# Performance work log

Measured on AMD Instinct MI355X. Metric: run time of the kernel, lower is better.

## Reference

```python
import jax, jax.numpy as jnp
import numpy as np

H = 8  # num_heads


def _ln(x, g, b):
    mu = x.mean(-1, keepdims=True)
    var = ((x - mu) ** 2).mean(-1, keepdims=True)
    return (x - mu) * jax.lax.rsqrt(var + 1e-5) * g + b


def setup_inputs() -> dict:
    key = jax.random.key(0)
    ks = jax.random.split(key, 24)
    B, N, V, E, D, R, L = 8, 512, 50000, 300, 256, 100, 4
    dh = D // H
    s = 0.02
    inp = {}
    inp['token_ids'] = jax.random.randint(ks[0], (B, N), 0, V, dtype=jnp.int32)
    inp['relations'] = jax.random.randint(ks[1], (B, N, N), 0, R, dtype=jnp.int32)
    m = jax.random.bernoulli(ks[2], 0.9, (B, N, N))
    eye = jnp.eye(N, dtype=bool)[None]
    inp['relations_mask'] = jnp.logical_or(m, eye)  # keep diagonal valid so every row attends somewhere
    inp['embed'] = jax.random.normal(ks[3], (V, E), jnp.float32) * s
    inp['W_in'] = jax.random.normal(ks[4], (E, D), jnp.float32) * s
    inp['b_in'] = jnp.zeros((D,), jnp.float32)
    inp['Wq'] = jax.random.normal(ks[5], (L, D, D), jnp.float32) * s
    inp['Wk'] = jax.random.normal(ks[6], (L, D, D), jnp.float32) * s
    inp['Wv'] = jax.random.normal(ks[7], (L, D, D), jnp.float32) * s
    inp['Wo'] = jax.random.normal(ks[8], (L, D, D), jnp.float32) * s
    inp['ln1_g'] = jnp.ones((L, D), jnp.float32)
    inp['ln1_b'] = jnp.zeros((L, D), jnp.float32)
    inp['ln2_g'] = jnp.ones((L, D), jnp.float32)
    inp['ln2_b'] = jnp.zeros((L, D), jnp.float32)
    inp['W1'] = jax.random.normal(ks[9], (L, D, 4 * D), jnp.float32) * s
    inp['b1'] = jnp.zeros((L, 4 * D), jnp.float32)
    inp['W2'] = jax.random.normal(ks[10], (L, 4 * D, D), jnp.float32) * s
    inp['b2'] = jnp.zeros((L, D), jnp.float32)
    inp['rel_k_emb'] = jax.random.normal(ks[11], (R, dh), jnp.float32) * s
    inp['rel_v_emb'] = jax.random.normal(ks[12], (R, dh), jnp.float32) * s
    inp['W_out'] = jax.random.normal(ks[13], (D, D), jnp.float32) * s
    inp['b_out'] = jnp.zeros((D,), jnp.float32)
    return inp


def reference(token_ids, relations, relations_mask, embed, W_in, b_in, Wq, Wk, Wv, Wo,
              ln1_g, ln1_b, ln2_g, ln2_b, W1, b1, W2, b2, rel_k_emb, rel_v_emb, W_out, b_out):
    # Input layer: embedding lookup + projection to gnn hidden size.
    x = embed[token_ids]                          # [B,N,E]
    x = jax.nn.relu(x @ W_in + b_in)              # [B,N,D]
    B, N, D = x.shape
    dh = D // H
    # Shared relation embeddings (share_layers=True, share_heads=True): gathered once.
    rk = rel_k_emb[relations]                     # [B,N,N,dh]
    rv = rel_v_emb[relations]                     # [B,N,N,dh]
    neg = jnp.asarray(-1e9, x.dtype)
    scale = jnp.asarray(1.0 / np.sqrt(dh), x.dtype)
    L = Wq.shape[0]
    for l in range(L):  # fixed small layer count
        q = (x @ Wq[l]).reshape(B, N, H, dh).transpose(0, 2, 1, 3)
        k = (x @ Wk[l]).reshape(B, N, H, dh).transpose(0, 2, 1, 3)
        v = (x @ Wv[l]).reshape(B, N, H, dh).transpose(0, 2, 1, 3)
        # Relation-aware scores: q.k + q.r_k (RAT-SQL)
        scores = (jnp.einsum('bhnd,bhmd->bhnm', q, k)
                  + jnp.einsum('bhnd,bnmd->bhnm', q, rk)) * scale
        scores = jnp.where(relations_mask[:, None], scores, neg)
        a = jax.nn.softmax(scores, axis=-1)       # [B,H,N,N]
        z = (jnp.einsum('bhnm,bhmd->bhnd', a, v)
             + jnp.einsum('bhnm,bnmd->bhnd', a, rv))
        z = z.transpose(0, 2, 1, 3).reshape(B, N, D) @ Wo[l]
        x = _ln(x + z, ln1_g[l], ln1_b[l])
        f = jax.nn.relu(x @ W1[l] + b1[l]) @ W2[l] + b2[l]
        x = _ln(x + f, ln2_g[l], ln2_b[l])
    # Output layer projection
    return x @ W_out + b_out
```

## Files before the change

### kernel.cpp

```cpp
#include <hip/hip_runtime.h>
#include <hip/hip_bf16.h>

#define NTOK 4096
#define NN   512

typedef __attribute__((ext_vector_type(8))) short bf16x8;
typedef __attribute__((ext_vector_type(4))) short bf16x4;
typedef __attribute__((ext_vector_type(4))) float f32x4;

__device__ __forceinline__ float bf16_to_f(unsigned short u) {
    unsigned int x = ((unsigned int)u) << 16;
    return __builtin_bit_cast(float, x);
}
__device__ __forceinline__ unsigned short f_to_bf16(float f) {
    unsigned int b = __builtin_bit_cast(unsigned int, f);
    return (unsigned short)((b + 0x7fff + ((b >> 16) & 1)) >> 16);
}
__device__ __forceinline__ bf16x8 pack8(float4 a, float4 b) {
    bf16x8 v;
    v[0]=(short)f_to_bf16(a.x); v[1]=(short)f_to_bf16(a.y);
    v[2]=(short)f_to_bf16(a.z); v[3]=(short)f_to_bf16(a.w);
    v[4]=(short)f_to_bf16(b.x); v[5]=(short)f_to_bf16(b.y);
    v[6]=(short)f_to_bf16(b.z); v[7]=(short)f_to_bf16(b.w);
    return v;
}

__global__ void detect_mask_kernel(const unsigned char* __restrict__ m, int* __restrict__ flag) {
    __shared__ int f;
    if (threadIdx.x == 0) f = 0;
    __syncthreads();
    int any = 0;
    for (int i = threadIdx.x; i < 4096; i += 256) {
        if ((i & 3) != 0 && m[i] != 0) any = 1;
    }
    if (any) atomicOr(&f, 1);
    __syncthreads();
    if (threadIdx.x == 0) *flag = f;
}

__global__ __launch_bounds__(256) void prep_rel16(
    const int* __restrict__ rel, const void* __restrict__ mask,
    const int* __restrict__ flag, short* __restrict__ rel16)
{
    const bool mbyte = (*flag != 0);
    const unsigned char* m8 = (const unsigned char*)mask;
    const int* m32 = (const int*)mask;
    const int i = (blockIdx.x * 256 + threadIdx.x) * 2;
    int2 rv = *(const int2*)(rel + i);
    int ok0, ok1;
    if (mbyte) { ok0 = m8[i]; ok1 = m8[i + 1]; }
    else       { ok0 = (m32[i] != 0); ok1 = (m32[i + 1] != 0); }
    short2 o;
    o.x = ok0 ? (short)rv.x : (short)-1;
    o.y = ok1 ? (short)rv.y : (short)-1;
    *(short2*)(rel16 + i) = o;
}

__global__ __launch_bounds__(256) void embed_proj_kernel(
    const int* __restrict__ tok, const float* __restrict__ embed,
    const float* __restrict__ W_in, const float* __restrict__ b_in,
    float* __restrict__ x)
{
    __shared__ float emb[8][304];
    __shared__ int tloc[8];
    const int t = threadIdx.x;
    const int r0 = blockIdx.x * 8;
    if (t < 8) tloc[t] = tok[r0 + t];
    __syncthreads();
    for (int i = t; i < 8 * 300; i += 256) {
        int r = i / 300, e = i - r * 300;
        emb[r][e] = embed[(size_t)tloc[r] * 300 + e];
    }
    __syncthreads();
    float acc[8] = {0.f,0.f,0.f,0.f,0.f,0.f,0.f,0.f};
    const int d = t;
    for (int e = 0; e < 300; ++e) {
        float w = W_in[e * 256 + d];
#pragma unroll
        for (int r = 0; r < 8; ++r) acc[r] += emb[r][e] * w;
    }
    const float bb = b_in[d];
#pragma unroll
    for (int r = 0; r < 8; ++r) {
        float o = acc[r] + bb;
        o = o > 0.f ? o : 0.f;
        x[(size_t)(r0 + r) * 256 + d] = o;
    }
}

__global__ __launch_bounds__(256) void gemm_mfma(
    const float* __restrict__ A,
    const float* __restrict__ W0, const float* __restrict__ W1p, const float* __restrict__ W2p,
    int ncPerW, const float* __restrict__ bias,
    float* __restrict__ C, int M, int K, int Nc, int relu)
{
    __shared__ unsigned short As[2][64][40];
    __shared__ unsigned short Bs[2][64][40];

    const int t = threadIdx.x;
    const int lane = t & 63, w = t >> 6;
    const int g = lane >> 4, li = lane & 15;
    const int r0 = blockIdx.y * 64, c0 = blockIdx.x * 64;

    const float* Wp = W0; int cW = c0;
    if (c0 >= 2 * ncPerW)      { Wp = W2p; cW = c0 - 2 * ncPerW; }
    else if (c0 >= ncPerW)     { Wp = W1p; cW = c0 - ncPerW; }

    f32x4 acc[4];
#pragma unroll
    for (int i = 0; i < 4; ++i) acc[i] = (f32x4){0.f, 0.f, 0.f, 0.f};

    const int arow = t >> 2, ad8 = (t & 3) * 8;
    const int bnn = t & 63, bk8 = (t >> 6) * 8;

    const float* ap0 = A + (size_t)(r0 + arow) * K + ad8;
    float4 a0 = *(const float4*)ap0;
    float4 a1 = *(const float4*)(ap0 + 4);
    float wv[8];
#pragma unroll
    for (int j = 0; j < 8; ++j)
        wv[j] = Wp[(size_t)(bk8 + j) * ncPerW + cW + bnn];

    const int nk = K >> 5;
    for (int ki = 0; ki < nk; ++ki) {
        const int cur = ki & 1;
        *(bf16x8*)&As[cur][arow][ad8] = pack8(a0, a1);
        {
            bf16x8 v;
#pragma unroll
            for (int j = 0; j < 8; ++j) v[j] = (short)f_to_bf16(wv[j]);
            *(bf16x8*)&Bs[cur][bnn][bk8] = v;
        }
        if (ki + 1 < nk) {
            const int k0 = (ki + 1) * 32;
            const float* ap = A + (size_t)(r0 + arow) * K + k0 + ad8;
            a0 = *(const float4*)ap;
            a1 = *(const float4*)(ap + 4);
#pragma unroll
            for (int j = 0; j < 8; ++j)
                wv[j] = Wp[(size_t)(k0 + bk8 + j) * ncPerW + cW + bnn];
        }
        __syncthreads();
        bf16x8 af = *(const bf16x8*)&As[cur][16 * w + li][g * 8];
#pragma unroll
        for (int sub = 0; sub < 4; ++sub) {
            bf16x8 bfr = *(const bf16x8*)&Bs[cur][16 * sub + li][g * 8];
            acc[sub] = __builtin_amdgcn_mfma_f32_16x16x32_bf16(af, bfr, acc[sub], 0, 0, 0);
        }
    }
#pragma unroll
    for (int sub = 0; sub < 4; ++sub) {
        int col = c0 + sub * 16 + li;
        float bv = bias ? bias[col] : 0.f;
#pragma unroll
        for (int r = 0; r < 4; ++r) {
            int row = r0 + 16 * w + g * 4 + r;
            float o = acc[sub][r] + bv;
            if (relu) o = fmaxf(o, 0.f);
            C[(size_t)row * Nc + col] = o;
        }
    }
}

__global__ __launch_bounds__(256, 3) void attn_mfma(
    const float* __restrict__ qkv,
    const short* __restrict__ rel16,
    const float* __restrict__ relk_g,
    const float* __restrict__ relv_g,
    float* __restrict__ zpart,
    float* __restrict__ smpart)
{
    const int p = blockIdx.x;
    const int cx = p & 7, kk = p >> 3;
    const int sg = cx * 32 + (kk >> 3);
    const int h  = kk & 7;
    const int b = sg >> 5, chunk = (sg >> 2) & 7, ms = sg & 3;
    const int n0 = chunk * 64, mbase = ms * 128;

    const int t = threadIdx.x;
    const int lane = t & 63, w = t >> 6;
    const int g = lane >> 4, li = lane & 15;
    const int qrow = 16 * w + g * 4;

    __shared__ float wrel[64][100];
    __shared__ unsigned short qrk[64][100];
    __shared__ union {
        unsigned short relk_s[100][40];
        unsigned short relvT[32][136];
        struct {
            unsigned short v_t[2][32][40];
            unsigned short p_s[4][16][40];
        } mn;
    } u;

    for (int i = t; i < 6400; i += 256) ((float*)wrel)[i] = 0.f;
    for (int i = t; i < 400; i += 256) {
        int rr = i >> 2, d8 = (i & 3) * 8;
        const float* sp = relk_g + rr * 32 + d8;
        *(bf16x8*)&u.relk_s[rr][d8] = pack8(*(const float4*)sp, *(const float4*)(sp + 4));
    }
    const float scale = 0.17677669529663687f;
    bf16x8 qf;
    {
        const float* qp = qkv + (size_t)(b * NN + n0 + 16 * w + li) * 768 + h * 32 + g * 8;
        float4 q0 = *(const float4*)qp, q1 = *(const float4*)(qp + 4);
        q0.x *= scale; q0.y *= scale; q0.z *= scale; q0.w *= scale;
        q1.x *= scale; q1.y *= scale; q1.z *= scale; q1.w *= scale;
        qf = pack8(q0, q1);
    }

    const short* relrow[4];
#pragma unroll
    for (int r = 0; r < 4; ++r)
        relrow[r] = rel16 + ((size_t)b * NN + n0 + qrow + r) * NN;
    const int vm = t & 31, vdg = t >> 5;
    const size_t kRB = (size_t)(b * NN) * 768 + 256 + h * 32 + g * 8;
    const size_t vRB = (size_t)(b * NN) * 768 + 512 + h * 32 + vdg * 4;

    float4 kld[4][4]; float4 vld[4]; short rld[4][8];
    {
        const int m0 = mbase;
        kld[0][0] = *(const float4*)(qkv + kRB + (size_t)(m0 + li) * 768);
        kld[0][1] = *(const float4*)(qkv + kRB + (size_t)(m0 + li) * 768 + 4);
        kld[0][2] = *(const float4*)(qkv + kRB + (size_t)(m0 + 16 + li) * 768);
        kld[0][3] = *(const float4*)(qkv + kRB + (size_t)(m0 + 16 + li) * 768 + 4);
        vld[0]    = *(const float4*)(qkv + vRB + (size_t)(m0 + vm) * 768);
#pragma unroll
        for (int idx = 0; idx < 8; ++idx)
            rld[0][idx] = relrow[idx & 3][m0 + (idx >> 2) * 16 + li];
    }
    __syncthreads();

#pragma unroll
    for (int rc = 0; rc < 7; ++rc) {
        bf16x8 bb = *(const bf16x8*)&u.relk_s[rc * 16 + li][g * 8];
        f32x4 s = __builtin_amdgcn_mfma_f32_16x16x32_bf16(qf, bb, (f32x4){0.f,0.f,0.f,0.f}, 0, 0, 0);
        int col = rc * 16 + li;
        if (col < 100) {
#pragma unroll
            for (int r = 0; r < 4; ++r)
                qrk[qrow + r][col] = f_to_bf16(s[r]);
        }
    }
    __syncthreads();

    float smacc[4] = {0.f, 0.f, 0.f, 0.f};
    f32x4 zf[2];
    zf[0] = (f32x4){0.f,0.f,0.f,0.f};
    zf[1] = (f32x4){0.f,0.f,0.f,0.f};

#pragma unroll
    for (int tt = 0; tt < 4; ++tt) {
        const int cur = tt & 1;
        {
            float4 vv = vld[tt];
            u.mn.v_t[cur][vdg * 4 + 0][vm] = f_to_bf16(vv.x);
            u.mn.v_t[cur][vdg * 4 + 1][vm] = f_to_bf16(vv.y);
            u.mn.v_t[cur][vdg * 4 + 2][vm] = f_to_bf16(vv.z);
            u.mn.v_t[cur][vdg * 4 + 3][vm] = f_to_bf16(vv.w);
        }
        __syncthreads();
        bf16x8 kf0 = pack8(kld[tt][0], kld[tt][1]);
        bf16x8 kf1 = pack8(kld[tt][2], kld[tt][3]);
        short rcur[8];
#pragma unroll
        for (int idx = 0; idx < 8; ++idx) rcur[idx] = rld[tt][idx];
        if (tt + 1 < 4) {
            const int m0n = mbase + (tt + 1) * 32;
            kld[tt+1][0] = *(const float4*)(qkv + kRB + (size_t)(m0n + li) * 768);
            kld[tt+1][1] = *(const float4*)(qkv + kRB + (size_t)(m0n + li) * 768 + 4);
            kld[tt+1][2] = *(const float4*)(qkv + kRB + (size_t)(m0n + 16 + li) * 768);
            kld[tt+1][3] = *(const float4*)(qkv + kRB + (size_t)(m0n + 16 + li) * 768 + 4);
            vld[tt+1]    = *(const float4*)(qkv + vRB + (size_t)(m0n + vm) * 768);
#pragma unroll
            for (int idx = 0; idx < 8; ++idx)
                rld[tt+1][idx] = relrow[idx & 3][m0n + (idx >> 2) * 16 + li];
        }
        f32x4 s0 = __builtin_amdgcn_mfma_f32_16x16x32_bf16(qf, kf0, (f32x4){0.f,0.f,0.f,0.f}, 0, 0, 0);
        f32x4 s1 = __builtin_amdgcn_mfma_f32_16x16x32_bf16(qf, kf1, (f32x4){0.f,0.f,0.f,0.f}, 0, 0, 0);
        float pr[8];
#pragma unroll
        for (int idx = 0; idx < 8; ++idx) {
            const int r = idx & 3;
            const int rl = rcur[idx];
            const int rla = rl < 0 ? 0 : rl;
            const float qadd = bf16_to_f(qrk[qrow + r][rla]);
            const float sv = ((idx >> 2) ? s1[r] : s0[r]) + qadd;
            float pv = 0.f;
            if (rl >= 0) {
                pv = __expf(fminf(sv, 50.f));
                atomicAdd(&wrel[qrow + r][rl], pv);
            }
            smacc[r] += pv;
            pr[idx] = pv;
        }
#pragma unroll
        for (int idx = 0; idx < 8; ++idx)
            u.mn.p_s[w][g * 4 + (idx & 3)][(idx >> 2) * 16 + li] = f_to_bf16(pr[idx]);

        asm volatile("s_waitcnt lgkmcnt(0)" ::: "memory");
        __builtin_amdgcn_sched_barrier(0);
        bf16x8 pa = *(const bf16x8*)&u.mn.p_s[w][li][g * 8];
#pragma unroll
        for (int dc = 0; dc < 2; ++dc) {
            bf16x8 vb = *(const bf16x8*)&u.mn.v_t[cur][dc * 16 + li][g * 8];
            zf[dc] = __builtin_amdgcn_mfma_f32_16x16x32_bf16(pa, vb, zf[dc], 0, 0, 0);
        }
    }
    __syncthreads();

    for (int i = t; i < 32 * 36; i += 256) {
        int d = i / 36, c = 100 + (i - (i / 36) * 36);
        u.relvT[d][c] = 0;
    }
    for (int i = t; i < 400; i += 256) {
        int rr2 = i >> 2, d8 = (i & 3) * 8;
        const float* sp = relv_g + rr2 * 32 + d8;
        float4 s0 = *(const float4*)sp, s1 = *(const float4*)(sp + 4);
        u.relvT[d8 + 0][rr2] = f_to_bf16(s0.x);
        u.relvT[d8 + 1][rr2] = f_to_bf16(s0.y);
        u.relvT[d8 + 2][rr2] = f_to_bf16(s0.z);
        u.relvT[d8 + 3][rr2] = f_to_bf16(s0.w);
        u.relvT[d8 + 4][rr2] = f_to_bf16(s1.x);
        u.relvT[d8 + 5][rr2] = f_to_bf16(s1.y);
        u.relvT[d8 + 6][rr2] = f_to_bf16(s1.z);
        u.relvT[d8 + 7][rr2] = f_to_bf16(s1.w);
    }
    __syncthreads();

#pragma unroll
    for (int kc = 0; kc < 4; ++kc) {
        const int kbase = kc * 32 + g * 8;
        const float* wp = &wrel[16 * w + li][0];
        bf16x8 af;
#pragma unroll
        for (int j = 0; j < 8; ++j) {
            int idx = kbase + j;
            float val = (idx < 100) ? wp[idx] : 0.f;
            af[j] = (short)f_to_bf16(val);
        }
#pragma unroll
        for (int dc = 0; dc < 2; ++dc) {
            bf16x8 vb = *(const bf16x8*)&u.relvT[dc * 16 + li][kbase];
            zf[dc] = __builtin_amdgcn_mfma_f32_16x16x32_bf16(af, vb, zf[dc], 0, 0, 0);
        }
    }

#pragma unroll
    for (int r = 0; r < 4; ++r) {
        smacc[r] += __shfl_xor(smacc[r], 1, 64);
        smacc[r] += __shfl_xor(smacc[r], 2, 64);
        smacc[r] += __shfl_xor(smacc[r], 4, 64);
        smacc[r] += __shfl_xor(smacc[r], 8, 64);
    }
#pragma unroll
    for (int r = 0; r < 4; ++r) {
        const int row = b * NN + n0 + qrow + r;
        size_t ob = (size_t)ms * 1048576 + (size_t)row * 256 + h * 32;
#pragma unroll
        for (int dc = 0; dc < 2; ++dc)
            zpart[ob + dc * 16 + li] = zf[dc][r];
        if (li == 0)
            smpart[(size_t)ms * 32768 + (size_t)row * 8 + h] = smacc[r];
    }
}

__global__ __launch_bounds__(256) void combine_kernel(
    const float* __restrict__ zpart, const float* __restrict__ smpart,
    float* __restrict__ z)
{
    const int t = threadIdx.x;
    const int wi = t >> 6, lane = t & 63;
    const int row = blockIdx.x * 4 + wi;
    const int h = lane >> 3;
    float den = 0.f;
    float4 acc = make_float4(0.f, 0.f, 0.f, 0.f);
#pragma unroll
    for (int s = 0; s < 4; ++s) {
        den += smpart[(size_t)s * 32768 + (size_t)row * 8 + h];
        float4 v = *(const float4*)(zpart + (size_t)s * 1048576 + (size_t)row * 256 + lane * 4);
        acc.x += v.x; acc.y += v.y; acc.z += v.z; acc.w += v.w;
    }
    const float inv = 1.f / den;
    acc.x *= inv; acc.y *= inv; acc.z *= inv; acc.w *= inv;
    *(float4*)(z + (size_t)row * 256 + lane * 4) = acc;
}

__global__ __launch_bounds__(256) void ln_kernel(
    const float* __restrict__ xin, const float* __restrict__ y,
    const float* __restrict__ g, const float* __restrict__ bsh,
    float* __restrict__ xout)
{
    const int t = threadIdx.x;
    const int w = t >> 6, lane = t & 63;
    const size_t row = (size_t)blockIdx.x * 4 + w;
    const float4 xv = *(const float4*)(xin + row * 256 + lane * 4);
    const float4 yv = *(const float4*)(y + row * 256 + lane * 4);
    float4 sv;
    sv.x = xv.x + yv.x; sv.y = xv.y + yv.y; sv.z = xv.z + yv.z; sv.w = xv.w + yv.w;
    float sum = sv.x + sv.y + sv.z + sv.w;
    float sq  = sv.x * sv.x + sv.y * sv.y + sv.z * sv.z + sv.w * sv.w;
#pragma unroll
    for (int off = 1; off < 64; off <<= 1) {
        sum += __shfl_xor(sum, off, 64);
        sq  += __shfl_xor(sq, off, 64);
    }
    const float mu = sum * (1.f / 256.f);
    const float var = sq * (1.f / 256.f) - mu * mu;
    const float rs = rsqrtf(var + 1e-5f);
    const float4 gv = *(const float4*)(g + lane * 4);
    const float4 bv = *(const float4*)(bsh + lane * 4);
    float4 o;
    o.x = (sv.x - mu) * rs * gv.x + bv.x;
    o.y = (sv.y - mu) * rs * gv.y + bv.y;
    o.z = (sv.z - mu) * rs * gv.z + bv.z;
    o.w = (sv.w - mu) * rs * gv.w + bv.w;
    *(float4*)(xout + row * 256 + lane * 4) = o;
}

extern "C" void kernel_launch(void* const* d_in, const int* in_sizes, int n_in,
                              void* d_out, int out_size, void* d_ws, size_t ws_size,
                              hipStream_t stream)
{
    (void)in_sizes; (void)n_in; (void)out_size;
    const int*   tok   = (const int*)d_in[0];
    const int*   rel   = (const int*)d_in[1];
    const void*  mask  = d_in[2];
    const float* embed = (const float*)d_in[3];
    const float* W_in  = (const float*)d_in[4];
    const float* b_in  = (const float*)d_in[5];
    const float* Wq    = (const float*)d_in[6];
    const float* Wk    = (const float*)d_in[7];
    const float* Wv    = (const float*)d_in[8];
    const float* Wo    = (const float*)d_in[9];
    const float* ln1g  = (const float*)d_in[10];
    const float* ln1b  = (const float*)d_in[11];
    const float* ln2g  = (const float*)d_in[12];
    const float* ln2b  = (const float*)d_in[13];
    const float* W1    = (const float*)d_in[14];
    const float* b1    = (const float*)d_in[15];
    const float* W2    = (const float*)d_in[16];
    const float* b2    = (const float*)d_in[17];
    const float* relk  = (const float*)d_in[18];
    const float* relv  = (const float*)d_in[19];
    const float* Wout  = (const float*)d_in[20];
    const float* bout  = (const float*)d_in[21];
    float* out = (float*)d_out;

    float* ws  = (float*)d_ws;
    float* x   = ws;
    float* z   = ws + (1u << 20);
    float* zo  = ws + 2u * (1u << 20);
    float* qkv = ws + 3u * (1u << 20);
    float* hb  = ws + 6u * (1u << 20);

    const bool roomy = ws_size >= ((size_t)45 << 20);
    short* rel16 = roomy ? (short*)(ws + 10u * (1u << 20)) : (short*)z;
    int*   flag  = (int*)(ws + (roomy ? 11u : 10u) * (1u << 20));
    float* zpart = hb;
    float* smpart = zo;

    detect_mask_kernel<<<1, 256, 0, stream>>>((const unsigned char*)mask, flag);
    if (roomy)
        prep_rel16<<<4096, 256, 0, stream>>>(rel, mask, flag, rel16);
    embed_proj_kernel<<<512, 256, 0, stream>>>(tok, embed, W_in, b_in, x);

    for (int l = 0; l < 4; ++l) {
        const float* wq = Wq + (size_t)l * 65536;
        const float* wk = Wk + (size_t)l * 65536;
        const float* wv = Wv + (size_t)l * 65536;
        const float* wo = Wo + (size_t)l * 65536;
        const float* w1 = W1 + (size_t)l * 262144;
        const float* w2 = W2 + (size_t)l * 262144;

        if (!roomy)
            prep_rel16<<<4096, 256, 0, stream>>>(rel, mask, flag, rel16);

        gemm_mfma<<<dim3(12, 64), 256, 0, stream>>>(x, wq, wk, wv, 256, nullptr,
                                                    qkv, NTOK, 256, 768, 0);
        attn_mfma<<<2048, 256, 0, stream>>>(qkv, rel16, relk, relv, zpart, smpart);
        combine_kernel<<<1024, 256, 0, stream>>>(zpart, smpart, z);
        gemm_mfma<<<dim3(4, 64), 256, 0, stream>>>(z, wo, wo, wo, 256, nullptr,
                                                   zo, NTOK, 256, 256, 0);
        ln_kernel<<<1024, 256, 0, stream>>>(x, zo, ln1g + l * 256, ln1b + l * 256, x);
        gemm_mfma<<<dim3(16, 64), 256, 0, stream>>>(x, w1, w1, w1, 1024, b1 + l * 1024,
                                                    hb, NTOK, 256, 1024, 1);
        gemm_mfma<<<dim3(4, 64), 256, 0, stream>>>(hb, w2, w2, w2, 256, b2 + l * 256,
                                                   zo, NTOK, 1024, 256, 0);
        ln_kernel<<<1024, 256, 0, stream>>>(x, zo, ln2g + l * 256, ln2b + l * 256, x);
    }
    gemm_mfma<<<dim3(4, 64), 256, 0, stream>>>(x, Wout, Wout, Wout, 256, bout,
                                               out, NTOK, 256, 256, 0);
}
```

Measured before the change: 702.8 us.

## Precompute q·relk globally, halve attention key splits, add 128-row GEMM tile

The per-block q·rel_k product moves out of the attention kernel into a separate qrk_kernel that writes bf16 results to a global buffer. Each attention block now covers 256 keys in 8 steps instead of 128 in 4, which halves the block count and lets combine_kernel sum 2 partials instead of 4. The attention kernel drops its qrk LDS table and asks for 4 blocks per SM. A new 128x64-tile GEMM is used for the QKV and FFN1 projections to improve operand reuse. The cost is an extra launch and a global gather of qrk values per score element, in place of an LDS lookup.

Result: no change. 705.9 us (+0.4%).

```diff
diff --git a/kernel.cpp b/kernel.cpp
--- a/kernel.cpp
+++ b/kernel.cpp
@@ -162,42 +162,105 @@
     }
 }
 
-__global__ __launch_bounds__(256, 3) void attn_mfma(
-    const float* __restrict__ qkv,
-    const short* __restrict__ rel16,
-    const float* __restrict__ relk_g,
-    const float* __restrict__ relv_g,
-    float* __restrict__ zpart,
-    float* __restrict__ smpart)
-{
-    const int p = blockIdx.x;
-    const int cx = p & 7, kk = p >> 3;
-    const int sg = cx * 32 + (kk >> 3);
-    const int h  = kk & 7;
-    const int b = sg >> 5, chunk = (sg >> 2) & 7, ms = sg & 3;
-    const int n0 = chunk * 64, mbase = ms * 128;
+__global__ __launch_bounds__(256) void gemm_mfma_128(
+    const float* __restrict__ A,
+    const float* __restrict__ W0, const float* __restrict__ W1p, const float* __restrict__ W2p,
+    int ncPerW, const float* __restrict__ bias,
+    float* __restrict__ C, int M, int K, int Nc, int relu)
+{
+    __shared__ unsigned short As[2][128][40];
+    __shared__ unsigned short Bs[2][64][40];
 
     const int t = threadIdx.x;
     const int lane = t & 63, w = t >> 6;
     const int g = lane >> 4, li = lane & 15;
+    const int r0 = blockIdx.y * 128, c0 = blockIdx.x * 64;
+
+    const float* Wp = W0; int cW = c0;
+    if (c0 >= 2 * ncPerW)      { Wp = W2p; cW = c0 - 2 * ncPerW; }
+    else if (c0 >= ncPerW)     { Wp = W1p; cW = c0 - ncPerW; }
+
+    f32x4 acc[2][4];
+#pragma unroll
+    for (int i = 0; i < 2; ++i)
+#pragma unroll
+        for (int j = 0; j < 4; ++j) acc[i][j] = (f32x4){0.f, 0.f, 0.f, 0.f};
+
+    const int arow = t >> 1, ah = (t & 1) * 16;
+    const int bnn = t & 63, bk8 = (t >> 6) * 8;
+
+    const float* ap0 = A + (size_t)(r0 + arow) * K + ah;
+    float4 a0 = *(const float4*)ap0;
+    float4 a1 = *(const float4*)(ap0 + 4);
+    float4 a2 = *(const float4*)(ap0 + 8);
+    float4 a3 = *(const float4*)(ap0 + 12);
+    float wv[8];
+#pragma unroll
+    for (int j = 0; j < 8; ++j)
+        wv[j] = Wp[(size_t)(bk8 + j) * ncPerW + cW + bnn];
+
+    const int nk = K >> 5;
+    for (int ki = 0; ki < nk; ++ki) {
+        const int cur = ki & 1;
+        *(bf16x8*)&As[cur][arow][ah]     = pack8(a0, a1);
+        *(bf16x8*)&As[cur][arow][ah + 8] = pack8(a2, a3);
+        {
+            bf16x8 v;
+#pragma unroll
+            for (int j = 0; j < 8; ++j) v[j] = (short)f_to_bf16(wv[j]);
+            *(bf16x8*)&Bs[cur][bnn][bk8] = v;
+        }
+        if (ki + 1 < nk) {
+            const int k0 = (ki + 1) * 32;
+            const float* ap = A + (size_t)(r0 + arow) * K + k0 + ah;
+            a0 = *(const float4*)ap;
+            a1 = *(const float4*)(ap + 4);
+            a2 = *(const float4*)(ap + 8);
+            a3 = *(const float4*)(ap + 12);
+#pragma unroll
+            for (int j = 0; j < 8; ++j)
+                wv[j] = Wp[(size_t)(k0 + bk8 + j) * ncPerW + cW + bnn];
+        }
+        __syncthreads();
+        bf16x8 af0 = *(const bf16x8*)&As[cur][32 * w + li][g * 8];
+        bf16x8 af1 = *(const bf16x8*)&As[cur][32 * w + 16 + li][g * 8];
+#pragma unroll
+        for (int sub = 0; sub < 4; ++sub) {
+            bf16x8 bfr = *(const bf16x8*)&Bs[cur][16 * sub + li][g * 8];
+            acc[0][sub] = __builtin_amdgcn_mfma_f32_16x16x32_bf16(af0, bfr, acc[0][sub], 0, 0, 0);
+            acc[1][sub] = __builtin_amdgcn_mfma_f32_16x16x32_bf16(af1, bfr, acc[1][sub], 0, 0, 0);
+        }
+    }
+#pragma unroll
+    for (int rc = 0; rc < 2; ++rc)
+#pragma unroll
+    for (int sub = 0; sub < 4; ++sub) {
+        int col = c0 + sub * 16 + li;
+        float bv = bias ? bias[col] : 0.f;
+#pragma unroll
+        for (int r = 0; r < 4; ++r) {
+            int row = r0 + 32 * w + rc * 16 + g * 4 + r;
+            float o = acc[rc][sub][r] + bv;
+            if (relu) o = fmaxf(o, 0.f);
+            C[(size_t)row * Nc + col] = o;
+        }
+    }
+}
+
+__global__ __launch_bounds__(256) void qrk_kernel(
+    const float* __restrict__ qkv, const float* __restrict__ relk_g,
+    unsigned short* __restrict__ qrkg)
+{
+    const int n0 = blockIdx.x * 64, h = blockIdx.y, b = blockIdx.z;
+    const int t = threadIdx.x, lane = t & 63, w = t >> 6;
+    const int g = lane >> 4, li = lane & 15;
     const int qrow = 16 * w + g * 4;
 
-    __shared__ float wrel[64][100];
-    __shared__ unsigned short qrk[64][100];
-    __shared__ union {
-        unsigned short relk_s[100][40];
-        unsigned short relvT[32][136];
-        struct {
-            unsigned short v_t[2][32][40];
-            unsigned short p_s[4][16][40];
-        } mn;
-    } u;
-
-    for (int i = t; i < 6400; i += 256) ((float*)wrel)[i] = 0.f;
+    __shared__ unsigned short relk_s[100][40];
     for (int i = t; i < 400; i += 256) {
         int rr = i >> 2, d8 = (i & 3) * 8;
         const float* sp = relk_g + rr * 32 + d8;
-        *(bf16x8*)&u.relk_s[rr][d8] = pack8(*(const float4*)sp, *(const float4*)(sp + 4));
+        *(bf16x8*)&relk_s[rr][d8] = pack8(*(const float4*)sp, *(const float4*)(sp + 4));
     }
     const float scale = 0.17677669529663687f;
     bf16x8 qf;
@@ -208,96 +271,148 @@
         q1.x *= scale; q1.y *= scale; q1.z *= scale; q1.w *= scale;
         qf = pack8(q0, q1);
     }
-
+    __syncthreads();
+#pragma unroll
+    for (int rc = 0; rc < 7; ++rc) {
+        bf16x8 bb = *(const bf16x8*)&relk_s[rc * 16 + li][g * 8];
+        f32x4 s = __builtin_amdgcn_mfma_f32_16x16x32_bf16(qf, bb, (f32x4){0.f,0.f,0.f,0.f}, 0, 0, 0);
+        int col = rc * 16 + li;
+        if (col < 100) {
+#pragma unroll
+            for (int r = 0; r < 4; ++r)
+                qrkg[((size_t)(b * 8 + h) * NN + n0 + qrow + r) * 100 + col] = f_to_bf16(s[r]);
+        }
+    }
+}
+
+__global__ __launch_bounds__(256, 4) void attn_mfma(
+    const float* __restrict__ qkv,
+    const short* __restrict__ rel16,
+    const unsigned short* __restrict__ qrkg,
+    const float* __restrict__ relv_g,
+    float* __restrict__ zpart,
+    float* __restrict__ smpart)
+{
+    const int p = blockIdx.x;
+    const int cx = p & 7, idx0 = p >> 3;
+    const int sg = cx * 8 + (idx0 >> 4);
+    const int hm = idx0 & 15;
+    const int h = hm >> 1, ms = hm & 1;
+    const int b = sg >> 3, chunk = sg & 7;
+    const int n0 = chunk * 64, mbase = ms * 256;
+
+    const int t = threadIdx.x;
+    const int lane = t & 63, w = t >> 6;
+    const int g = lane >> 4, li = lane & 15;
+    const int qrow = 16 * w + g * 4;
+
+    __shared__ float wrel[64][100];
+    __shared__ union {
+        unsigned short relvT[32][136];
+        struct {
+            unsigned short v_t[2][32][40];
+            unsigned short p_s[4][16][40];
+        } mn;
+    } u;
+
+    for (int i = t; i < 6400; i += 256) ((float*)wrel)[i] = 0.f;
+    const float scale = 0.17677669529663687f;
+    bf16x8 qf;
+    {
+        const float* qp = qkv + (size_t)(b * NN + n0 + 16 * w + li) * 768 + h * 32 + g * 8;
+        float4 q0 = *(const float4*)qp, q1 = *(const float4*)(qp + 4);
+        q0.x *= scale; q0.y *= scale; q0.z *= scale; q0.w *= scale;
+        q1.x *= scale; q1.y *= scale; q1.z *= scale; q1.w *= scale;
+        qf = pack8(q0, q1);
+    }
     const short* relrow[4];
-#pragma unroll
-    for (int r = 0; r < 4; ++r)
+    const unsigned short* qgr[4];
+#pragma unroll
+    for (int r = 0; r < 4; ++r) {
         relrow[r] = rel16 + ((size_t)b * NN + n0 + qrow + r) * NN;
+        qgr[r] = qrkg + ((size_t)(b * 8 + h) * NN + n0 + qrow + r) * 100;
+    }
     const int vm = t & 31, vdg = t >> 5;
     const size_t kRB = (size_t)(b * NN) * 768 + 256 + h * 32 + g * 8;
     const size_t vRB = (size_t)(b * NN) * 768 + 512 + h * 32 + vdg * 4;
 
-    float4 kld[4][4]; float4 vld[4]; short rld[4][8];
+    float4 kbuf[2][4]; float4 vbuf[2];
+    short rbuf[2][8]; unsigned short qvb[2][8];
     {
-        const int m0 = mbase;
-        kld[0][0] = *(const float4*)(qkv + kRB + (size_t)(m0 + li) * 768);
-        kld[0][1] = *(const float4*)(qkv + kRB + (size_t)(m0 + li) * 768 + 4);
-        kld[0][2] = *(const float4*)(qkv + kRB + (size_t)(m0 + 16 + li) * 768);
-        kld[0][3] = *(const float4*)(qkv + kRB + (size_t)(m0 + 16 + li) * 768 + 4);
-        vld[0]    = *(const float4*)(qkv + vRB + (size_t)(m0 + vm) * 768);
-#pragma unroll
-        for (int idx = 0; idx < 8; ++idx)
-            rld[0][idx] = relrow[idx & 3][m0 + (idx >> 2) * 16 + li];
-    }
-    __syncthreads();
-
-#pragma unroll
-    for (int rc = 0; rc < 7; ++rc) {
-        bf16x8 bb = *(const bf16x8*)&u.relk_s[rc * 16 + li][g * 8];
-        f32x4 s = __builtin_amdgcn_mfma_f32_16x16x32_bf16(qf, bb, (f32x4){0.f,0.f,0.f,0.f}, 0, 0, 0);
-        int col = rc * 16 + li;
-        if (col < 100) {
-#pragma unroll
-            for (int r = 0; r < 4; ++r)
-                qrk[qrow + r][col] = f_to_bf16(s[r]);
-        }
-    }
-    __syncthreads();
-
+#pragma unroll
+        for (int i = 0; i < 8; ++i)
+            rbuf[0][i] = relrow[i & 3][mbase + (i >> 2) * 16 + li];
+        kbuf[0][0] = *(const float4*)(qkv + kRB + (size_t)(mbase + li) * 768);
+        kbuf[0][1] = *(const float4*)(qkv + kRB + (size_t)(mbase + li) * 768 + 4);
+        kbuf[0][2] = *(const float4*)(qkv + kRB + (size_t)(mbase + 16 + li) * 768);
+        kbuf[0][3] = *(const float4*)(qkv + kRB + (size_t)(mbase + 16 + li) * 768 + 4);
+        vbuf[0]    = *(const float4*)(qkv + vRB + (size_t)(mbase + vm) * 768);
+#pragma unroll
+        for (int i = 0; i < 8; ++i) {
+            int rl = rbuf[0][i];
+            qvb[0][i] = qgr[i & 3][rl < 0 ? 0 : rl];
+        }
+    }
     float smacc[4] = {0.f, 0.f, 0.f, 0.f};
     f32x4 zf[2];
     zf[0] = (f32x4){0.f,0.f,0.f,0.f};
     zf[1] = (f32x4){0.f,0.f,0.f,0.f};
 
-#pragma unroll
-    for (int tt = 0; tt < 4; ++tt) {
-        const int cur = tt & 1;
+    __syncthreads();
+
+#pragma unroll
+    for (int tt = 0; tt < 8; ++tt) {
+        const int cur = tt & 1, nxt = cur ^ 1;
         {
-            float4 vv = vld[tt];
+            float4 vv = vbuf[cur];
             u.mn.v_t[cur][vdg * 4 + 0][vm] = f_to_bf16(vv.x);
             u.mn.v_t[cur][vdg * 4 + 1][vm] = f_to_bf16(vv.y);
             u.mn.v_t[cur][vdg * 4 + 2][vm] = f_to_bf16(vv.z);
             u.mn.v_t[cur][vdg * 4 + 3][vm] = f_to_bf16(vv.w);
         }
+        if (tt + 1 < 8) {
+            const int m0n = mbase + (tt + 1) * 32;
+#pragma unroll
+            for (int i = 0; i < 8; ++i)
+                rbuf[nxt][i] = relrow[i & 3][m0n + (i >> 2) * 16 + li];
+        }
         __syncthreads();
-        bf16x8 kf0 = pack8(kld[tt][0], kld[tt][1]);
-        bf16x8 kf1 = pack8(kld[tt][2], kld[tt][3]);
-        short rcur[8];
-#pragma unroll
-        for (int idx = 0; idx < 8; ++idx) rcur[idx] = rld[tt][idx];
-        if (tt + 1 < 4) {
+        bf16x8 kf0 = pack8(kbuf[cur][0], kbuf[cur][1]);
+        bf16x8 kf1 = pack8(kbuf[cur][2], kbuf[cur][3]);
+        if (tt + 1 < 8) {
             const int m0n = mbase + (tt + 1) * 32;
-            kld[tt+1][0] = *(const float4*)(qkv + kRB + (size_t)(m0n + li) * 768);
-            kld[tt+1][1] = *(const float4*)(qkv + kRB + (size_t)(m0n + li) * 768 + 4);
-            kld[tt+1][2] = *(const float4*)(qkv + kRB + (size_t)(m0n + 16 + li) * 768);
-            kld[tt+1][3] = *(const float4*)(qkv + kRB + (size_t)(m0n + 16 + li) * 768 + 4);
-            vld[tt+1]    = *(const float4*)(qkv + vRB + (size_t)(m0n + vm) * 768);
-#pragma unroll
-            for (int idx = 0; idx < 8; ++idx)
-                rld[tt+1][idx] = relrow[idx & 3][m0n + (idx >> 2) * 16 + li];
+            kbuf[nxt][0] = *(const float4*)(qkv + kRB + (size_t)(m0n + li) * 768);
+            kbuf[nxt][1] = *(const float4*)(qkv + kRB + (size_t)(m0n + li) * 768 + 4);
+            kbuf[nxt][2] = *(const float4*)(qkv + kRB + (size_t)(m0n + 16 + li) * 768);
+            kbuf[nxt][3] = *(const float4*)(qkv + kRB + (size_t)(m0n + 16 + li) * 768 + 4);
+            vbuf[nxt]    = *(const float4*)(qkv + vRB + (size_t)(m0n + vm) * 768);
         }
         f32x4 s0 = __builtin_amdgcn_mfma_f32_16x16x32_bf16(qf, kf0, (f32x4){0.f,0.f,0.f,0.f}, 0, 0, 0);
         f32x4 s1 = __builtin_amdgcn_mfma_f32_16x16x32_bf16(qf, kf1, (f32x4){0.f,0.f,0.f,0.f}, 0, 0, 0);
         float pr[8];
 #pragma unroll
-        for (int idx = 0; idx < 8; ++idx) {
-            const int r = idx & 3;
-            const int rl = rcur[idx];
-            const int rla = rl < 0 ? 0 : rl;
-            const float qadd = bf16_to_f(qrk[qrow + r][rla]);
-            const float sv = ((idx >> 2) ? s1[r] : s0[r]) + qadd;
+        for (int i = 0; i < 8; ++i) {
+            const int r = i & 3;
+            const int rl = rbuf[cur][i];
+            const float sv = ((i >> 2) ? s1[r] : s0[r]) + bf16_to_f(qvb[cur][i]);
             float pv = 0.f;
             if (rl >= 0) {
                 pv = __expf(fminf(sv, 50.f));
                 atomicAdd(&wrel[qrow + r][rl], pv);
             }
             smacc[r] += pv;
-            pr[idx] = pv;
-        }
-#pragma unroll
-        for (int idx = 0; idx < 8; ++idx)
-            u.mn.p_s[w][g * 4 + (idx & 3)][(idx >> 2) * 16 + li] = f_to_bf16(pr[idx]);
-
+            pr[i] = pv;
+        }
+#pragma unroll
+        for (int i = 0; i < 8; ++i)
+            u.mn.p_s[w][g * 4 + (i & 3)][(i >> 2) * 16 + li] = f_to_bf16(pr[i]);
+        if (tt + 1 < 8) {
+#pragma unroll
+            for (int i = 0; i < 8; ++i) {
+                int rl = rbuf[nxt][i];
+                qvb[nxt][i] = qgr[i & 3][rl < 0 ? 0 : rl];
+            }
+        }
         asm volatile("s_waitcnt lgkmcnt(0)" ::: "memory");
         __builtin_amdgcn_sched_barrier(0);
         bf16x8 pa = *(const bf16x8*)&u.mn.p_s[w][li][g * 8];
@@ -335,8 +450,8 @@
         bf16x8 af;
 #pragma unroll
         for (int j = 0; j < 8; ++j) {
-            int idx = kbase + j;
-            float val = (idx < 100) ? wp[idx] : 0.f;
+            int id = kbase + j;
+            float val = (id < 100) ? wp[id] : 0.f;
             af[j] = (short)f_to_bf16(val);
         }
 #pragma unroll
@@ -376,7 +491,7 @@
     float den = 0.f;
     float4 acc = make_float4(0.f, 0.f, 0.f, 0.f);
 #pragma unroll
-    for (int s = 0; s < 4; ++s) {
+    for (int s = 0; s < 2; ++s) {
         den += smpart[(size_t)s * 32768 + (size_t)row * 8 + h];
         float4 v = *(const float4*)(zpart + (size_t)s * 1048576 + (size_t)row * 256 + lane * 4);
         acc.x += v.x; acc.y += v.y; acc.z += v.z; acc.w += v.w;
@@ -458,6 +573,7 @@
     short* rel16 = roomy ? (short*)(ws + 10u * (1u << 20)) : (short*)z;
     int*   flag  = (int*)(ws + (roomy ? 11u : 10u) * (1u << 20));
     float* zpart = hb;
+    unsigned short* qrkg = (unsigned short*)(hb + 2u * (1u << 20));
     float* smpart = zo;
 
     detect_mask_kernel<<<1, 256, 0, stream>>>((const unsigned char*)mask, flag);
@@ -476,15 +592,16 @@
         if (!roomy)
             prep_rel16<<<4096, 256, 0, stream>>>(rel, mask, flag, rel16);
 
-        gemm_mfma<<<dim3(12, 64), 256, 0, stream>>>(x, wq, wk, wv, 256, nullptr,
-                                                    qkv, NTOK, 256, 768, 0);
-        attn_mfma<<<2048, 256, 0, stream>>>(qkv, rel16, relk, relv, zpart, smpart);
+        gemm_mfma_128<<<dim3(12, 32), 256, 0, stream>>>(x, wq, wk, wv, 256, nullptr,
+                                                        qkv, NTOK, 256, 768, 0);
+        qrk_kernel<<<dim3(8, 8, 8), 256, 0, stream>>>(qkv, relk, qrkg);
+        attn_mfma<<<1024, 256, 0, stream>>>(qkv, rel16, qrkg, relv, zpart, smpart);
         combine_kernel<<<1024, 256, 0, stream>>>(zpart, smpart, z);
         gemm_mfma<<<dim3(4, 64), 256, 0, stream>>>(z, wo, wo, wo, 256, nullptr,
                                                    zo, NTOK, 256, 256, 0);
         ln_kernel<<<1024, 256, 0, stream>>>(x, zo, ln1g + l * 256, ln1b + l * 256, x);
-        gemm_mfma<<<dim3(16, 64), 256, 0, stream>>>(x, w1, w1, w1, 1024, b1 + l * 1024,
-                                                    hb, NTOK, 256, 1024, 1);
+        gemm_mfma_128<<<dim3(16, 32), 256, 0, stream>>>(x, w1, w1, w1, 1024, b1 + l * 1024,
+                                                        hb, NTOK, 256, 1024, 1);
         gemm_mfma<<<dim3(4, 64), 256, 0, stream>>>(hb, w2, w2, w2, 256, b2 + l * 256,
                                                    zo, NTOK, 1024, 256, 0);
         ln_kernel<<<1024, 256, 0, stream>>>(x, zo, ln2g + l * 256, ln2b + l * 256, x);
```
